# Optimization experiments

Hardware: AMD Instinct MI355X
Metric: run time of the kernel (lower is better)

Reference implementation:

```python
import jax, jax.numpy as jnp
import numpy as np
from jax import lax

NUM_BLOCKS = 8
BLOCK = 4  # hidden_size 32 // num_blocks 8
LAMBDA = 0.01  # sparsity_threshold
BN_EPS = 1e-5


def _bn(x, gamma, beta):
    # training-mode BatchNorm2d over (N, H, W) per channel
    mean = jnp.mean(x, axis=(0, 2, 3), keepdims=True)
    var = jnp.var(x, axis=(0, 2, 3), keepdims=True)
    return gamma[None, :, None, None] * (x - mean) * lax.rsqrt(var + BN_EPS) + beta[None, :, None, None]


def _softshrink(x, lam):
    return jnp.where(x > lam, x - lam, jnp.where(x < -lam, x + lam, jnp.zeros_like(x)))


def _afno(x, w1, b1, w2, b2):
    # AFNO2D_channelfirst: rfft2 -> block-diagonal complex 2-layer MLP -> softshrink
    # -> multiply with original spectrum -> irfft2 -> residual add
    B, C, H, W = x.shape
    bias = x
    xf = jnp.fft.rfft2(x, axes=(2, 3), norm="ortho")          # [B, C, H, W//2+1] complex
    orig = xf
    Wf = xf.shape[-1]
    xb = xf.reshape(B, NUM_BLOCKS, BLOCK, H, Wf)
    xr, xi = jnp.real(xb), jnp.imag(xb)
    # layer 1 (complex block matmul + bias + ReLU)
    o1r = jax.nn.relu(jnp.einsum('bkihw,kio->bkohw', xr, w1[0])
                      - jnp.einsum('bkihw,kio->bkohw', xi, w1[1])
                      + b1[0][None, :, :, None, None])
    o1i = jax.nn.relu(jnp.einsum('bkihw,kio->bkohw', xi, w1[0])
                      + jnp.einsum('bkihw,kio->bkohw', xr, w1[1])
                      + b1[1][None, :, :, None, None])
    # layer 2
    o2r = (jnp.einsum('bkihw,kio->bkohw', o1r, w2[0])
           - jnp.einsum('bkihw,kio->bkohw', o1i, w2[1])
           + b2[0][None, :, :, None, None])
    o2i = (jnp.einsum('bkihw,kio->bkohw', o1i, w2[0])
           + jnp.einsum('bkihw,kio->bkohw', o1r, w2[1])
           + b2[1][None, :, :, None, None])
    o2r = _softshrink(o2r, LAMBDA)
    o2i = _softshrink(o2i, LAMBDA)
    z = (o2r + 1j * o2i).reshape(B, C, H, Wf)
    z = z * orig                                              # spectral gating by original spectrum
    out = jnp.fft.irfft2(z, s=(H, W), axes=(2, 3), norm="ortho")
    return out + bias


def setup_inputs() -> dict:
    key = jax.random.key(0)
    ks = jax.random.split(key, 6)
    return {
        "x": jax.random.normal(ks[0], (4, 32, 512, 512), jnp.float32),
        "conv_w": jax.random.normal(ks[1], (32, 32, 3, 3), jnp.float32) * 0.05,
        "conv_b": jnp.zeros((32,), jnp.float32),
        "bn1_gamma": jnp.ones((32,), jnp.float32),
        "bn1_beta": jnp.zeros((32,), jnp.float32),
        "w1": jax.random.normal(ks[2], (2, NUM_BLOCKS, BLOCK, BLOCK), jnp.float32) * 0.02,
        "b1": jax.random.normal(ks[3], (2, NUM_BLOCKS, BLOCK), jnp.float32) * 0.02,
        "w2": jax.random.normal(ks[4], (2, NUM_BLOCKS, BLOCK, BLOCK), jnp.float32) * 0.02,
        "b2": jax.random.normal(ks[5], (2, NUM_BLOCKS, BLOCK), jnp.float32) * 0.02,
        "bn2_gamma": jnp.ones((32,), jnp.float32),
        "bn2_beta": jnp.zeros((32,), jnp.float32),
    }


def reference(x, conv_w, conv_b, bn1_gamma, bn1_beta, w1, b1, w2, b2, bn2_gamma, bn2_beta):
    # conv1 = Conv3x3(norm=True, act=True): conv 3x3 pad 1 + BN + ReLU
    y = lax.conv_general_dilated(x, conv_w, (1, 1), ((1, 1), (1, 1)),
                                 dimension_numbers=('NCHW', 'OIHW', 'NCHW'))
    y = y + conv_b[None, :, None, None]
    y = jax.nn.relu(_bn(y, bn1_gamma, bn1_beta))
    fo = _afno(y, w1, b1, w2, b2)
    fo = _bn(fo, bn2_gamma, bn2_beta)
    return jax.nn.relu(y + fo)
```

## Files before the change

### kernel.cpp

```cpp
#include <hip/hip_runtime.h>

#define WF 257
#define LAM 0.01f
#define ROWH 540
#define LPH(i) ((i) + (((i)>>6)<<2))

#define WSYNC() do { asm volatile("" ::: "memory"); __builtin_amdgcn_wave_barrier(); asm volatile("" ::: "memory"); } while(0)

typedef __attribute__((ext_vector_type(8))) short short8;
typedef __attribute__((ext_vector_type(4))) float f32x4;
typedef __attribute__((ext_vector_type(2))) __fp16 h2v;

__device__ __forceinline__ ushort f2bf(float f){
    unsigned u = __float_as_uint(f);
    unsigned r = (u + 0x7fffu + ((u >> 16) & 1u)) >> 16;
    return (ushort)r;
}
__device__ __forceinline__ float bf2f(ushort u){ return __uint_as_float((uint)u << 16); }
__device__ __forceinline__ uint packbf(float a, float b){
    return (uint)f2bf(a) | ((uint)f2bf(b) << 16);
}
__device__ __forceinline__ float2 unpackbf(uint u){
    return make_float2(__uint_as_float(u << 16), __uint_as_float(u & 0xffff0000u));
}
__device__ __forceinline__ uint packh(float a, float b){
    h2v h = __builtin_amdgcn_cvt_pkrtz(a, b);
    return *(uint*)&h;
}
__device__ __forceinline__ uint packh2(float2 v){ return packh(v.x, v.y); }
__device__ __forceinline__ float2 unph(uint u){
    h2v h = *(h2v*)&u;
    return make_float2((float)h[0], (float)h[1]);
}

__device__ __forceinline__ float2 cmul(float2 a, float2 b){
    return make_float2(a.x*b.x - a.y*b.y, a.x*b.y + a.y*b.x);
}
__device__ __forceinline__ float2 cadd(float2 a, float2 b){ return make_float2(a.x+b.x, a.y+b.y); }
__device__ __forceinline__ float2 csub(float2 a, float2 b){ return make_float2(a.x-b.x, a.y-b.y); }

template<int NTHREADS>
__device__ __forceinline__ void ld_tw(float2* tw, const float2* __restrict__ twg, int tid){
    for (int t = tid; t < 256; t += NTHREADS)
        ((float4*)tw)[t] = ((const float4*)twg)[t];
}

template<bool INV>
__device__ __forceinline__ float2 twz(const float2* tw, int idx){
    float2 w = tw[idx];
    if (INV) w.y = -w.y;
    return w;
}

template<bool INV>
__device__ __forceinline__ void dft8(float2 v[8]) {
    const float R = 0.70710678118654752f;
    float2 y0=v[0], y1=v[4], y2=v[2], y3=v[6], y4=v[1], y5=v[5], y6=v[3], y7=v[7];
    float2 t;
    t=y1; y1=csub(y0,t); y0=cadd(y0,t);
    t=y3; y3=csub(y2,t); y2=cadd(y2,t);
    t=y5; y5=csub(y4,t); y4=cadd(y4,t);
    t=y7; y7=csub(y6,t); y6=cadd(y6,t);
    t=y2; y2=csub(y0,t); y0=cadd(y0,t);
    t = INV ? make_float2(-y3.y, y3.x) : make_float2(y3.y, -y3.x);
    y3=csub(y1,t); y1=cadd(y1,t);
    t=y6; y6=csub(y4,t); y4=cadd(y4,t);
    t = INV ? make_float2(-y7.y, y7.x) : make_float2(y7.y, -y7.x);
    y7=csub(y5,t); y5=cadd(y5,t);
    t=y4; y4=csub(y0,t); y0=cadd(y0,t);
    { float2 w8 = INV ? make_float2(R, R) : make_float2(R,-R);
      t=cmul(y5,w8); y5=csub(y1,t); y1=cadd(y1,t); }
    t = INV ? make_float2(-y6.y, y6.x) : make_float2(y6.y, -y6.x);
    y6=csub(y2,t); y2=cadd(y2,t);
    { float2 w8 = INV ? make_float2(-R, R) : make_float2(-R,-R);
      t=cmul(y7,w8); y7=csub(y3,t); y3=cadd(y3,t); }
    v[0]=y0; v[1]=y1; v[2]=y2; v[3]=y3; v[4]=y4; v[5]=y5; v[6]=y6; v[7]=y7;
}

__device__ __forceinline__ void oct_write(uint* drow, int l, const float2 v[8]){
    uint* p = drow + LPH(8*l);
    *(uint4*)p       = make_uint4(packh2(v[0]), packh2(v[1]), packh2(v[2]), packh2(v[3]));
    *(uint4*)(p + 4) = make_uint4(packh2(v[4]), packh2(v[5]), packh2(v[6]), packh2(v[7]));
}

__device__ __forceinline__ void oct_gather(const uint* drow, int o0, float2 v[8]){
    const uint* b = drow + LPH(o0);
    #pragma unroll
    for (int q = 0; q < 8; ++q) v[q] = unph(b[68*q]);
}

template<bool INV>
__device__ __forceinline__ void fft_wave12(uint* drow, const float2* tw, int l)
{
    WSYNC();
    {
        int a = l&7, m = l>>3;
        uint* b = drow + 68*m + a;
        float2 v[8];
        v[0] = unph(b[0]);
        #pragma unroll
        for (int j = 1; j < 8; ++j)
            v[j] = cmul(unph(b[8*j]), twz<INV>(tw, 8*a*j));
        dft8<INV>(v);
        #pragma unroll
        for (int j = 0; j < 8; ++j) b[8*j] = packh2(v[j]);
    }
    WSYNC();
    {
        uint* b = drow + l;
        float2 v[8];
        v[0] = unph(b[0]);
        #pragma unroll
        for (int q = 1; q < 8; ++q)
            v[q] = cmul(unph(b[68*q]), twz<INV>(tw, (l*q)&511));
        dft8<INV>(v);
        #pragma unroll
        for (int q = 0; q < 8; ++q) b[68*q] = packh2(v[q]);
    }
    WSYNC();
}

__global__ void k_twiddle(float2* __restrict__ twg){
    int t = blockIdx.x*256 + threadIdx.x;
    if (t < 512) {
        float s, c;
        sincosf((float)t * (-6.2831853071795864769f/512.0f), &s, &c);
        twg[t] = make_float2(c, s);
    }
}

__global__ void k_wprep(const float* __restrict__ w, ushort* __restrict__ wtp){
    int i = blockIdx.x*256 + threadIdx.x;
    if (i < 9216) {
        int j = i & 7, l = (i>>3) & 63, m = (i>>9) & 1, tap = i >> 10;
        int co = m*16 + (l & 15), ci = ((l>>4)&3)*8 + j;
        wtp[i] = f2bf(w[(co*32 + ci)*9 + tap]);
    }
}

__global__ __launch_bounds__(256) void k_transpose(const float* __restrict__ x, ushort* __restrict__ xt){
    __shared__ ushort tl[64][36];
    const int tid = threadIdx.x;
    const int w0 = blockIdx.x*64, h = blockIdx.y, b = blockIdx.z;
    #pragma unroll
    for (int it = 0; it < 8; ++it) {
        int i = it*256 + tid, c = i >> 6, ww = i & 63;
        tl[ww][c] = f2bf(x[(((size_t)b*32 + c)*512 + h)*512 + w0 + ww]);
    }
    __syncthreads();
    const int ww = tid >> 2, c0 = (tid & 3) * 8;
    uint4 v;
    v.x = *(const uint*)&tl[ww][c0+0];
    v.y = *(const uint*)&tl[ww][c0+2];
    v.z = *(const uint*)&tl[ww][c0+4];
    v.w = *(const uint*)&tl[ww][c0+6];
    *(uint4*)(xt + ((((size_t)b*512 + h)*512 + w0 + ww)*32 + c0)) = v;
}

__global__ __launch_bounds__(256) void k_conv_mfma(
    const ushort* __restrict__ xt, const ushort* __restrict__ wtp,
    const float* __restrict__ bias, ushort* __restrict__ out, float* __restrict__ stats)
{
    __shared__ float sred[64];
    const int tid = threadIdx.x;
    const int wid = tid >> 6, lane = tid & 63;
    const int h = blockIdx.y*4 + wid;
    const int w0 = blockIdx.x*64;
    const int b = blockIdx.z;

    short8 wa[9][2];
    #pragma unroll
    for (int tap = 0; tap < 9; ++tap)
        #pragma unroll
        for (int m = 0; m < 2; ++m)
            wa[tap][m] = *reinterpret_cast<const short8*>(wtp + ((tap*2 + m)*64 + lane)*8);

    f32x4 acc[2][4];
    #pragma unroll
    for (int m = 0; m < 2; ++m)
        #pragma unroll
        for (int n = 0; n < 4; ++n)
            acc[m][n] = (f32x4){0.f, 0.f, 0.f, 0.f};

    const int c0 = ((lane >> 4) & 3) * 8;
    const int pw = w0 + (lane & 15);
    const size_t ibase = (size_t)b * 512 * 512;

    #pragma unroll
    for (int dy = -1; dy <= 1; ++dy) {
        const int hh = h + dy;
        const bool hok = (unsigned)hh < 512u;
        #pragma unroll
        for (int dx = -1; dx <= 1; ++dx) {
            const int tap = (dy+1)*3 + (dx+1);
            short8 bfr[4];
            #pragma unroll
            for (int n = 0; n < 4; ++n) {
                const int ww = pw + n*16 + dx;
                short8 v = {0,0,0,0,0,0,0,0};
                if (hok && (unsigned)ww < 512u)
                    v = *reinterpret_cast<const short8*>(xt + ((ibase + (size_t)hh*512 + ww)*32 + c0));
                bfr[n] = v;
            }
            #pragma unroll
            for (int m = 0; m < 2; ++m)
                #pragma unroll
                for (int n = 0; n < 4; ++n)
                    acc[m][n] = __builtin_amdgcn_mfma_f32_16x16x32_bf16(wa[tap][m], bfr[n], acc[m][n], 0, 0, 0);
        }
    }

    if (tid < 64) sred[tid] = 0.f;
    __syncthreads();

    float bv[2][4];
    #pragma unroll
    for (int m = 0; m < 2; ++m)
        #pragma unroll
        for (int r = 0; r < 4; ++r)
            bv[m][r] = bias[m*16 + ((lane>>4)&3)*4 + r];

    float s8[8], q8[8];
    #pragma unroll
    for (int i = 0; i < 8; ++i) { s8[i] = 0.f; q8[i] = 0.f; }

    #pragma unroll
    for (int m = 0; m < 2; ++m) {
        #pragma unroll
        for (int n = 0; n < 4; ++n) {
            #pragma unroll
            for (int r = 0; r < 4; ++r) {
                const int co = m*16 + ((lane>>4)&3)*4 + r;
                const int ww = w0 + n*16 + (lane & 15);
                float val = acc[m][n][r] + bv[m][r];
                out[(((size_t)b*32 + co)*512 + h)*512 + ww] = f2bf(val);
                s8[m*4+r] += val;
                q8[m*4+r] += val*val;
            }
        }
    }
    #pragma unroll
    for (int i = 0; i < 8; ++i) {
        #pragma unroll
        for (int off = 1; off < 16; off <<= 1) {
            s8[i] += __shfl_xor(s8[i], off, 64);
            q8[i] += __shfl_xor(q8[i], off, 64);
        }
    }
    if ((lane & 15) == 0) {
        #pragma unroll
        for (int m = 0; m < 2; ++m)
            #pragma unroll
            for (int r = 0; r < 4; ++r) {
                const int co = m*16 + ((lane>>4)&3)*4 + r;
                atomicAdd(&sred[co], s8[m*4+r]);
                atomicAdd(&sred[32+co], q8[m*4+r]);
            }
    }
    __syncthreads();
    if (tid < 64) {
        int bin = (blockIdx.y*8 + blockIdx.x + blockIdx.z) & 63;
        atomicAdd(&stats[bin*64 + tid], sred[tid]);
    }
}

__global__ void k_finalize(const float* __restrict__ stats, int nbins, const float* __restrict__ g,
                           const float* __restrict__ bta, float* __restrict__ bnp)
{
    int c = threadIdx.x;
    if (c < 32) {
        float s = 0.f, q = 0.f;
        for (int i = 0; i < nbins; ++i) { s += stats[i*64 + c]; q += stats[i*64 + 32 + c]; }
        const float inv_n = 1.f/1048576.f;
        float mean = s * inv_n;
        float var  = q * inv_n - mean*mean;
        float sc = g[c] * rsqrtf(var + 1e-5f);
        bnp[c] = sc;
        bnp[32+c] = bta[c] - mean*sc;
    }
}

__global__ void k_finalize2(const float* __restrict__ ystats, const float* __restrict__ sstats,
                            const float* __restrict__ g, const float* __restrict__ bta,
                            float* __restrict__ bnp2)
{
    int c = threadIdx.x;
    if (c < 32) {
        float Sy = 0.f, Sy2 = 0.f, Sgg = 0.f, Sgu = 0.f, Sg0 = 0.f;
        for (int i = 0; i < 64; ++i){ Sy  += ystats[i*64 + c]; Sy2 += ystats[i*64 + 32 + c]; }
        for (int i = 0; i < 32; ++i){ Sgg += sstats[i*96 + c]; Sgu += sstats[i*96 + 32 + c]; Sg0 += sstats[i*96 + 64 + c]; }
        const float inv_n = 1.f/1048576.f;
        float Sfo  = Sg0 + Sy;
        float Sfo2 = Sgg*(1.f/512.f) + Sgu*(2.f/512.f) + Sy2;
        float mean = Sfo*inv_n;
        float var  = Sfo2*inv_n - mean*mean;
        float sc = g[c]*rsqrtf(var + 1e-5f);
        bnp2[c] = sc;
        bnp2[32+c] = bta[c] - mean*sc;
    }
}

__global__ __launch_bounds__(512) void k_rowfft_fwd(
    const ushort* __restrict__ cvo, const float* __restrict__ bnp,
    const float2* __restrict__ twg, uint* __restrict__ spec, float* __restrict__ ystats)
{
    __shared__ float2 tw[512];
    __shared__ uint d[8*ROWH];
    const int tid = threadIdx.x;
    const int h0 = blockIdx.x * 16;
    const int bc = blockIdx.y;
    const int c = bc & 31;
    ld_tw<512>(tw, twg, tid);
    __syncthreads();
    const float s1 = bnp[c], t1 = bnp[32+c];
    const int row = tid >> 6, l = tid & 63;
    const int o0 = ((l&7)<<3) | (l>>3);
    uint* drow = d + row*ROWH;
    const ushort* rp0 = cvo + ((size_t)bc*512 + h0 + 2*row)*512 + o0;
    const ushort* rp1 = rp0 + 512;
    float ls = 0.f, lsq = 0.f;
    float2 v[8];
    #pragma unroll
    for (int q = 0; q < 8; ++q) {
        float y0 = fmaxf(fmaf(bf2f(rp0[64*q]), s1, t1), 0.f);
        float y1 = fmaxf(fmaf(bf2f(rp1[64*q]), s1, t1), 0.f);
        ls += y0 + y1; lsq += y0*y0 + y1*y1;
        v[q] = make_float2(y0, y1);
    }
    dft8<false>(v);
    oct_write(drow, l, v);
    fft_wave12<false>(drow, tw, l);
    __syncthreads();
    for (int i = tid; i < 8*WF; i += 512) {
        int p = i & 7, w = i >> 3;
        float2 Z  = unph(d[p*ROWH + LPH(w)]);
        float2 Zm = unph(d[p*ROWH + LPH((512 - w) & 511)]);
        float x1r = 0.5f*(Z.x + Zm.x), x1i = 0.5f*(Z.y - Zm.y);
        float x2r = 0.5f*(Z.y + Zm.y), x2i = 0.5f*(Zm.x - Z.x);
        uint2 pk;
        pk.x = packbf(x1r, x1i);
        pk.y = packbf(x2r, x2i);
        *(uint2*)(spec + ((size_t)bc*WF + w)*512 + h0 + 2*p) = pk;
    }
    #pragma unroll
    for (int off = 32; off; off >>= 1){ ls += __shfl_down(ls, off, 64); lsq += __shfl_down(lsq, off, 64); }
    if (l == 0) {
        int bin = ((blockIdx.x << 3) + row) & 63;
        atomicAdd(&ystats[bin*64 + c], ls);
        atomicAdd(&ystats[bin*64 + 32 + c], lsq);
    }
}

__global__ __launch_bounds__(512) void k_colfft(uint* __restrict__ spec,
    const float* __restrict__ w1, const float* __restrict__ b1,
    const float* __restrict__ w2, const float* __restrict__ b2,
    const float2* __restrict__ twg, float* __restrict__ sstats)
{
    __shared__ float2 tw[512];
    __shared__ uint d[8*ROWH];
    __shared__ float wl[160];
    const int tid = threadIdx.x;
    const int w = blockIdx.x;
    const int by = blockIdx.y;
    const int b = blockIdx.z;
    ld_tw<512>(tw, twg, tid);
    if (tid < 32) {
        int kg = tid >> 4, j = tid & 15;
        int k = by*2 + kg;
        wl[kg*80 + j]      = w1[k*16 + j];
        wl[kg*80 + 16 + j] = w1[128 + k*16 + j];
        wl[kg*80 + 32 + j] = w2[k*16 + j];
        wl[kg*80 + 48 + j] = w2[128 + k*16 + j];
    } else if (tid < 40) {
        int t = tid - 32, kg = t >> 2, o = t & 3;
        int k = by*2 + kg;
        wl[kg*80 + 64 + o] = b1[k*4 + o];
        wl[kg*80 + 68 + o] = b1[32 + k*4 + o];
        wl[kg*80 + 72 + o] = b2[k*4 + o];
        wl[kg*80 + 76 + o] = b2[32 + k*4 + o];
    }
    __syncthreads();
    const int cc = tid >> 6, l = tid & 63;
    const int o0 = ((l&7)<<3) | (l>>3);
    uint* drow = d + cc*ROWH;
    const size_t cbase = ((size_t)(b*32 + by*8 + cc)*WF + w) * 512;
    {
        const uint* sp = spec + cbase + o0;
        float2 v[8];
        #pragma unroll
        for (int q = 0; q < 8; ++q) {
            float2 u = unpackbf(sp[64*q]);
            v[q] = make_float2(u.x*(1.f/512.f), u.y*(1.f/512.f));
        }
        dft8<false>(v);
        oct_write(drow, l, v);
    }
    fft_wave12<false>(drow, tw, l);
    __syncthreads();
    const int ph = LPH(tid);
    #pragma unroll
    for (int kg = 0; kg < 2; ++kg) {
        const float* wk = wl + kg*80;
        const int rb = kg*4;
        float xr[4], xi[4];
        #pragma unroll
        for (int i = 0; i < 4; ++i) {
            float2 vv = unph(d[(rb+i)*ROWH + ph]);
            xr[i] = vv.x;
            xi[i] = vv.y;
        }
        float o1r[4], o1i[4];
        #pragma unroll
        for (int o = 0; o < 4; ++o) {
            float sr = wk[64+o], si = wk[68+o];
            #pragma unroll
            for (int i = 0; i < 4; ++i) {
                float wr = wk[i*4+o], wi = wk[16 + i*4+o];
                sr += xr[i]*wr - xi[i]*wi;
                si += xi[i]*wr + xr[i]*wi;
            }
            o1r[o] = fmaxf(sr, 0.f);
            o1i[o] = fmaxf(si, 0.f);
        }
        #pragma unroll
        for (int o = 0; o < 4; ++o) {
            float sr = wk[72+o], si = wk[76+o];
            #pragma unroll
            for (int i = 0; i < 4; ++i) {
                float wr = wk[32 + i*4+o], wi = wk[48 + i*4+o];
                sr += o1r[i]*wr - o1i[i]*wi;
                si += o1i[i]*wr + o1r[i]*wi;
            }
            sr = (sr > LAM) ? sr - LAM : ((sr < -LAM) ? sr + LAM : 0.f);
            si = (si > LAM) ? si - LAM : ((si < -LAM) ? si + LAM : 0.f);
            d[(rb+o)*ROWH + ph] = packh(sr*xr[o] - si*xi[o], sr*xi[o] + si*xr[o]);
        }
    }
    __syncthreads();
    {
        float2 v[8];
        oct_gather(drow, o0, v);
        dft8<true>(v);
        WSYNC();
        oct_write(drow, l, v);
    }
    fft_wave12<true>(drow, tw, l);
    const bool edge = (w == 0) || (w == 256);
    float fgg = 0.f, fgu = 0.f, fg0 = 0.f;
    #pragma unroll
    for (int it = 0; it < 4; ++it) {
        const int pos = it*64 + l;
        uint2 up = *(const uint2*)(spec + cbase + 2*pos);
        float2 u0 = unpackbf(up.x), u1 = unpackbf(up.y);
        uint2 dv = *(const uint2*)(drow + LPH(2*pos));
        float2 z0 = unph(dv.x), z1 = unph(dv.y);
        uint2 gp;
        gp.x = packbf(z0.x, z0.y);
        gp.y = packbf(z1.x, z1.y);
        *(uint2*)(spec + cbase + 2*pos) = gp;
        float2 g0 = unpackbf(gp.x), g1 = unpackbf(gp.y);
        if (edge) {
            fgg += g0.x*g0.x + g1.x*g1.x;
            fgu += g0.x*u0.x + g1.x*u1.x;
            if (w == 0) fg0 += g0.x + g1.x;
        } else {
            fgg += 2.f*(g0.x*g0.x + g0.y*g0.y + g1.x*g1.x + g1.y*g1.y);
            fgu += 2.f*(g0.x*u0.x + g0.y*u0.y + g1.x*u1.x + g1.y*u1.y);
        }
    }
    #pragma unroll
    for (int off = 32; off; off >>= 1){
        fgg += __shfl_down(fgg, off, 64);
        fgu += __shfl_down(fgu, off, 64);
        fg0 += __shfl_down(fg0, off, 64);
    }
    if (l == 0) {
        int kk = by*2 + (cc >> 2);
        int ch = cc & 3;
        int bin = (w + b*8 + kk) & 31;
        atomicAdd(&sstats[bin*96 + kk*4 + ch], fgg);
        atomicAdd(&sstats[bin*96 + 32 + kk*4 + ch], fgu);
        if (w == 0) atomicAdd(&sstats[bin*96 + 64 + kk*4 + ch], fg0);
    }
}

__global__ __launch_bounds__(512) void k_rowfft_inv(
    const uint* __restrict__ spec, const ushort* __restrict__ cvo,
    const float* __restrict__ bnp, const float* __restrict__ bnp2,
    const float2* __restrict__ twg, float* __restrict__ out)
{
    __shared__ float2 tw[512];
    __shared__ uint d[8*ROWH];
    const int tid = threadIdx.x;
    const int h0 = blockIdx.x * 16;
    const int bc = blockIdx.y;
    const int c = bc & 31;
    ld_tw<512>(tw, twg, tid);
    for (int i = tid; i < 8*WF; i += 512) {
        int p = i & 7, w = i >> 3;
        uint2 pk = *(const uint2*)(spec + ((size_t)bc*WF + w)*512 + h0 + 2*p);
        float2 X1 = unpackbf(pk.x), X2 = unpackbf(pk.y);
        if (w == 0 || w == 256) { X1.y = 0.f; X2.y = 0.f; }
        const float s = 1.f/512.f;
        d[p*ROWH + LPH(w)] = packh((X1.x - X2.y)*s, (X1.y + X2.x)*s);
        if ((unsigned)(w - 1) < 255u)
            d[p*ROWH + LPH(512 - w)] = packh((X1.x + X2.y)*s, (X2.x - X1.y)*s);
    }
    __syncthreads();
    const int row = tid >> 6, l = tid & 63;
    const int o0 = ((l&7)<<3) | (l>>3);
    uint* drow = d + row*ROWH;
    {
        float2 v[8];
        oct_gather(drow, o0, v);
        dft8<true>(v);
        WSYNC();
        oct_write(drow, l, v);
    }
    fft_wave12<true>(drow, tw, l);
    const float s1 = bnp[c],  t1 = bnp[32+c];
    const float s2 = bnp2[c], t2 = bnp2[32+c];
    const size_t gbase = ((size_t)bc*512 + h0 + 2*row)*512;
    #pragma unroll
    for (int q = 0; q < 8; ++q) {
        const int col = q*64 + l;
        float2 v = unph(drow[LPH(col)]);
        float y0 = fmaxf(fmaf(bf2f(cvo[gbase + col]), s1, t1), 0.f);
        float fo0 = v.x + y0;
        out[gbase + col] = fmaxf(y0 + fmaf(fo0, s2, t2), 0.f);
        float y1 = fmaxf(fmaf(bf2f(cvo[gbase + 512 + col]), s1, t1), 0.f);
        float fo1 = v.y + y1;
        out[gbase + 512 + col] = fmaxf(y1 + fmaf(fo1, s2, t2), 0.f);
    }
}

extern "C" void kernel_launch(void* const* d_in, const int* in_sizes, int n_in,
                              void* d_out, int out_size, void* d_ws, size_t ws_size,
                              hipStream_t stream)
{
    const float* x      = (const float*)d_in[0];
    const float* conv_w = (const float*)d_in[1];
    const float* conv_b = (const float*)d_in[2];
    const float* bn1g   = (const float*)d_in[3];
    const float* bn1b   = (const float*)d_in[4];
    const float* w1     = (const float*)d_in[5];
    const float* b1     = (const float*)d_in[6];
    const float* w2     = (const float*)d_in[7];
    const float* b2     = (const float*)d_in[8];
    const float* bn2g   = (const float*)d_in[9];
    const float* bn2b   = (const float*)d_in[10];
    float* out = (float*)d_out;

    char* ws = (char*)d_ws;
    uint*   spec  = (uint*)ws;
    ushort* xt    = (ushort*)ws;
    ushort* cvo   = (ushort*)(ws + 67371008);
    ushort* wtp   = (ushort*)(ws + 67371008 + 67108864);
    float*  stats = (float*)(ws + 67371008 + 67108864 + 18432);
    float* stats1 = stats;
    float* ystats = stats + 4096;
    float* sstats = stats + 8192;
    float* bnp1   = stats + 11264;
    float* bnp2   = stats + 11328;
    float2* twg   = (float2*)(stats + 11392);

    (void)hipMemsetAsync(stats, 0, 11264*sizeof(float), stream);
    k_twiddle<<<2, 256, 0, stream>>>(twg);
    k_wprep<<<36, 256, 0, stream>>>(conv_w, wtp);
    k_transpose<<<dim3(8,512,4), 256, 0, stream>>>(x, xt);
    k_conv_mfma<<<dim3(8,128,4), 256, 0, stream>>>(xt, wtp, conv_b, cvo, stats1);
    k_finalize<<<1, 64, 0, stream>>>(stats1, 64, bn1g, bn1b, bnp1);
    k_rowfft_fwd<<<dim3(32,128), 512, 0, stream>>>(cvo, bnp1, twg, spec, ystats);
    k_colfft<<<dim3(257,4,4), 512, 0, stream>>>(spec, w1, b1, w2, b2, twg, sstats);
    k_finalize2<<<1, 64, 0, stream>>>(ystats, sstats, bn2g, bn2b, bnp2);
    k_rowfft_inv<<<dim3(32,128), 512, 0, stream>>>(spec, cvo, bnp1, bnp2, twg, out);
}
```

Before: 357.7 us.

## Compute column FFTs as fp16 MFMA DFT matmuls over all 32 channels per block

Replaces the radix-8 shared-memory column FFT in k_colfft with a two-stage 16x32 decomposition done as complex DFT matrix multiplies on fp16 MFMA units, forward and inverse. Each block now handles all 32 channels of one frequency column, so the grid shrinks from 257x4x4 to 257x4 and the block-MLP runs over all 8 channel groups at once. The aim is to move butterfly arithmetic and the twiddle and permutation shuffles onto matrix cores. In exchange it uses about 66 KB of LDS per block, which lowers occupancy, has half-idle lanes in the 16-point stage, and adds fp16 rounding inside the DFT.

```diff
diff --git a/kernel.cpp b/kernel.cpp
--- a/kernel.cpp
+++ b/kernel.cpp
@@ -10,6 +10,9 @@
 typedef __attribute__((ext_vector_type(8))) short short8;
 typedef __attribute__((ext_vector_type(4))) float f32x4;
 typedef __attribute__((ext_vector_type(2))) __fp16 h2v;
+typedef __attribute__((ext_vector_type(8))) __fp16 h8;
+
+union UH8 { uint4 u; h8 h; };
 
 __device__ __forceinline__ ushort f2bf(float f){
     unsigned u = __float_as_uint(f);
@@ -356,58 +359,153 @@
     const float* __restrict__ w2, const float* __restrict__ b2,
     const float2* __restrict__ twg, float* __restrict__ sstats)
 {
+    __shared__ uint sl[32*513];
     __shared__ float2 tw[512];
-    __shared__ uint d[8*ROWH];
-    __shared__ float wl[160];
+    __shared__ float wl[640];
     const int tid = threadIdx.x;
-    const int w = blockIdx.x;
-    const int by = blockIdx.y;
-    const int b = blockIdx.z;
-    ld_tw<512>(tw, twg, tid);
-    if (tid < 32) {
-        int kg = tid >> 4, j = tid & 15;
-        int k = by*2 + kg;
-        wl[kg*80 + j]      = w1[k*16 + j];
-        wl[kg*80 + 16 + j] = w1[128 + k*16 + j];
-        wl[kg*80 + 32 + j] = w2[k*16 + j];
-        wl[kg*80 + 48 + j] = w2[128 + k*16 + j];
-    } else if (tid < 40) {
-        int t = tid - 32, kg = t >> 2, o = t & 3;
-        int k = by*2 + kg;
-        wl[kg*80 + 64 + o] = b1[k*4 + o];
-        wl[kg*80 + 68 + o] = b1[32 + k*4 + o];
-        wl[kg*80 + 72 + o] = b2[k*4 + o];
-        wl[kg*80 + 76 + o] = b2[32 + k*4 + o];
-    }
-    __syncthreads();
-    const int cc = tid >> 6, l = tid & 63;
-    const int o0 = ((l&7)<<3) | (l>>3);
-    uint* drow = d + cc*ROWH;
-    const size_t cbase = ((size_t)(b*32 + by*8 + cc)*WF + w) * 512;
+    const int lane = tid & 63, wv = tid >> 6;
+    const int w = blockIdx.x, b = blockIdx.y;
+    const int l15 = lane & 15, lq = lane >> 4;
+    const int kb = lq * 8;
+
+    for (int t = tid; t < 256; t += 512)
+        ((float4*)tw)[t] = ((const float4*)twg)[t];
+    if (tid < 128) {
+        int g = tid >> 4, j = tid & 15;
+        wl[g*80 + j]      = w1[g*16 + j];
+        wl[g*80 + 16 + j] = w1[128 + g*16 + j];
+        wl[g*80 + 32 + j] = w2[g*16 + j];
+        wl[g*80 + 48 + j] = w2[128 + g*16 + j];
+    } else if (tid < 160) {
+        int t2 = tid - 128, g = t2 >> 2, o = t2 & 3;
+        wl[g*80 + 64 + o] = b1[g*4 + o];
+        wl[g*80 + 68 + o] = b1[32 + g*4 + o];
+        wl[g*80 + 72 + o] = b2[g*4 + o];
+        wl[g*80 + 76 + o] = b2[32 + g*4 + o];
+    }
+    const size_t gbase = ((size_t)b*32*WF + w) * 512;
+    #pragma unroll 4
+    for (int c = 0; c < 32; ++c) {
+        float2 u = unpackbf(spec[gbase + (size_t)c*(WF*512) + tid]);
+        sl[c*513 + tid] = packh(u.x*(1.f/512.f), u.y*(1.f/512.f));
+    }
+    __syncthreads();
+
     {
-        const uint* sp = spec + cbase + o0;
-        float2 v[8];
-        #pragma unroll
-        for (int q = 0; q < 8; ++q) {
-            float2 u = unpackbf(sp[64*q]);
-            v[q] = make_float2(u.x*(1.f/512.f), u.y*(1.f/512.f));
-        }
-        dft8<false>(v);
-        oct_write(drow, l, v);
-    }
-    fft_wave12<false>(drow, tw, l);
-    __syncthreads();
-    const int ph = LPH(tid);
-    #pragma unroll
-    for (int kg = 0; kg < 2; ++kg) {
-        const float* wk = wl + kg*80;
-        const int rb = kg*4;
+        h8 Fr[2], Fi[2], nFi[2];
+        #pragma unroll
+        for (int mt = 0; mt < 2; ++mt) {
+            const int m = mt*16 + l15;
+            uint ur[4], ui[4], un[4];
+            #pragma unroll
+            for (int p = 0; p < 4; ++p) {
+                float2 t0 = tw[(16*m*(kb + 2*p)) & 511];
+                float2 t1 = tw[(16*m*(kb + 2*p+1)) & 511];
+                ur[p] = packh(t0.x, t1.x);
+                ui[p] = packh(t0.y, t1.y);
+                un[p] = ui[p] ^ 0x80008000u;
+            }
+            UH8 a; a.u = make_uint4(ur[0],ur[1],ur[2],ur[3]); Fr[mt]=a.h;
+            UH8 bb; bb.u = make_uint4(ui[0],ui[1],ui[2],ui[3]); Fi[mt]=bb.h;
+            UH8 cc; cc.u = make_uint4(un[0],un[1],un[2],un[3]); nFi[mt]=cc.h;
+        }
+        #pragma unroll
+        for (int s = 0; s < 2; ++s) {
+            const int n1 = wv*2 + s;
+            h8 Br[2], Bi[2];
+            #pragma unroll
+            for (int nt = 0; nt < 2; ++nt) {
+                const int base = (nt*16 + l15)*513 + n1;
+                uint dd[8];
+                #pragma unroll
+                for (int j = 0; j < 8; ++j) dd[j] = sl[base + 16*(kb + j)];
+                uint br[4], bi[4];
+                #pragma unroll
+                for (int p = 0; p < 4; ++p) {
+                    br[p] = (dd[2*p] & 0xffffu) | (dd[2*p+1] << 16);
+                    bi[p] = (dd[2*p] >> 16) | (dd[2*p+1] & 0xffff0000u);
+                }
+                UH8 t1_; t1_.u = make_uint4(br[0],br[1],br[2],br[3]); Br[nt]=t1_.h;
+                UH8 t2_; t2_.u = make_uint4(bi[0],bi[1],bi[2],bi[3]); Bi[nt]=t2_.h;
+            }
+            #pragma unroll
+            for (int mt = 0; mt < 2; ++mt)
+            #pragma unroll
+            for (int nt = 0; nt < 2; ++nt) {
+                f32x4 yr = {0.f,0.f,0.f,0.f}, yi = {0.f,0.f,0.f,0.f};
+                yr = __builtin_amdgcn_mfma_f32_16x16x32_f16(Fr[mt], Br[nt], yr, 0,0,0);
+                yr = __builtin_amdgcn_mfma_f32_16x16x32_f16(nFi[mt], Bi[nt], yr, 0,0,0);
+                yi = __builtin_amdgcn_mfma_f32_16x16x32_f16(Fr[mt], Bi[nt], yi, 0,0,0);
+                yi = __builtin_amdgcn_mfma_f32_16x16x32_f16(Fi[mt], Br[nt], yi, 0,0,0);
+                const int cw = (nt*16 + l15)*513 + n1;
+                #pragma unroll
+                for (int r = 0; r < 4; ++r)
+                    sl[cw + 16*(mt*16 + lq*4 + r)] = packh(yr[r], yi[r]);
+            }
+        }
+    }
+    __syncthreads();
+
+    #pragma unroll
+    for (int s = 0; s < 4; ++s) {
+        const int k2 = wv*4 + s;
+        h8 Ar, Ai, nAi;
+        {
+            uint ar[4]={0,0,0,0}, ai[4]={0,0,0,0}, an[4]={0,0,0,0};
+            if (lane < 32) {
+                const int kk = k2 + 32*l15;
+                #pragma unroll
+                for (int p = 0; p < 4; ++p) {
+                    float2 t0 = tw[((kb + 2*p)*kk) & 511];
+                    float2 t1 = tw[((kb + 2*p+1)*kk) & 511];
+                    ar[p] = packh(t0.x, t1.x);
+                    ai[p] = packh(t0.y, t1.y);
+                    an[p] = ai[p] ^ 0x80008000u;
+                }
+            }
+            UH8 a; a.u = make_uint4(ar[0],ar[1],ar[2],ar[3]); Ar=a.h;
+            UH8 bb; bb.u = make_uint4(ai[0],ai[1],ai[2],ai[3]); Ai=bb.h;
+            UH8 cc; cc.u = make_uint4(an[0],an[1],an[2],an[3]); nAi=cc.h;
+        }
+        #pragma unroll
+        for (int ct = 0; ct < 2; ++ct) {
+            const int cb2 = (ct*16 + l15)*513 + 16*k2;
+            h8 Br, Bi;
+            {
+                uint dd[8] = {0,0,0,0,0,0,0,0};
+                if (lane < 32) {
+                    #pragma unroll
+                    for (int j = 0; j < 8; ++j) dd[j] = sl[cb2 + kb + j];
+                }
+                uint br[4], bi[4];
+                #pragma unroll
+                for (int p = 0; p < 4; ++p) {
+                    br[p] = (dd[2*p] & 0xffffu) | (dd[2*p+1] << 16);
+                    bi[p] = (dd[2*p] >> 16) | (dd[2*p+1] & 0xffff0000u);
+                }
+                UH8 t1_; t1_.u = make_uint4(br[0],br[1],br[2],br[3]); Br=t1_.h;
+                UH8 t2_; t2_.u = make_uint4(bi[0],bi[1],bi[2],bi[3]); Bi=t2_.h;
+            }
+            f32x4 xr = {0.f,0.f,0.f,0.f}, xi = {0.f,0.f,0.f,0.f};
+            xr = __builtin_amdgcn_mfma_f32_16x16x32_f16(Ar, Br, xr, 0,0,0);
+            xr = __builtin_amdgcn_mfma_f32_16x16x32_f16(nAi, Bi, xr, 0,0,0);
+            xi = __builtin_amdgcn_mfma_f32_16x16x32_f16(Ar, Bi, xi, 0,0,0);
+            xi = __builtin_amdgcn_mfma_f32_16x16x32_f16(Ai, Br, xi, 0,0,0);
+            #pragma unroll
+            for (int r = 0; r < 4; ++r)
+                sl[cb2 + lq*4 + r] = packh(xr[r], xi[r]);
+        }
+    }
+    __syncthreads();
+
+    #pragma unroll
+    for (int g = 0; g < 8; ++g) {
+        const float* wk = wl + g*80;
         float xr[4], xi[4];
         #pragma unroll
         for (int i = 0; i < 4; ++i) {
-            float2 vv = unph(d[(rb+i)*ROWH + ph]);
-            xr[i] = vv.x;
-            xi[i] = vv.y;
+            float2 v = unph(sl[(4*g+i)*513 + tid]);
+            xr[i] = v.x; xi[i] = v.y;
         }
         float o1r[4], o1i[4];
         #pragma unroll
@@ -433,54 +531,159 @@
             }
             sr = (sr > LAM) ? sr - LAM : ((sr < -LAM) ? sr + LAM : 0.f);
             si = (si > LAM) ? si - LAM : ((si < -LAM) ? si + LAM : 0.f);
-            d[(rb+o)*ROWH + ph] = packh(sr*xr[o] - si*xi[o], sr*xi[o] + si*xr[o]);
-        }
-    }
-    __syncthreads();
+            sl[(4*g+o)*513 + tid] = packh(sr*xr[o] - si*xi[o], sr*xi[o] + si*xr[o]);
+        }
+    }
+    __syncthreads();
+
     {
-        float2 v[8];
-        oct_gather(drow, o0, v);
-        dft8<true>(v);
-        WSYNC();
-        oct_write(drow, l, v);
-    }
-    fft_wave12<true>(drow, tw, l);
+        h8 Gr, Gi, nGi;
+        {
+            uint gr[4]={0,0,0,0}, gi[4]={0,0,0,0}, gn[4]={0,0,0,0};
+            if (lane < 32) {
+                #pragma unroll
+                for (int p = 0; p < 4; ++p) {
+                    float2 t0 = tw[(32*(kb + 2*p)*l15) & 511];
+                    float2 t1 = tw[(32*(kb + 2*p+1)*l15) & 511];
+                    gr[p] = packh(t0.x, t1.x);
+                    gi[p] = packh(-t0.y, -t1.y);
+                    gn[p] = gi[p] ^ 0x80008000u;
+                }
+            }
+            UH8 a; a.u = make_uint4(gr[0],gr[1],gr[2],gr[3]); Gr=a.h;
+            UH8 bb; bb.u = make_uint4(gi[0],gi[1],gi[2],gi[3]); Gi=bb.h;
+            UH8 cc; cc.u = make_uint4(gn[0],gn[1],gn[2],gn[3]); nGi=cc.h;
+        }
+        #pragma unroll
+        for (int s = 0; s < 4; ++s) {
+            const int k2 = wv*4 + s;
+            #pragma unroll
+            for (int ct = 0; ct < 2; ++ct) {
+                const int cb2 = (ct*16 + l15)*513 + 16*k2;
+                h8 Br, Bi;
+                {
+                    uint dd[8] = {0,0,0,0,0,0,0,0};
+                    if (lane < 32) {
+                        #pragma unroll
+                        for (int j = 0; j < 8; ++j) dd[j] = sl[cb2 + kb + j];
+                    }
+                    uint br[4], bi[4];
+                    #pragma unroll
+                    for (int p = 0; p < 4; ++p) {
+                        br[p] = (dd[2*p] & 0xffffu) | (dd[2*p+1] << 16);
+                        bi[p] = (dd[2*p] >> 16) | (dd[2*p+1] & 0xffff0000u);
+                    }
+                    UH8 t1_; t1_.u = make_uint4(br[0],br[1],br[2],br[3]); Br=t1_.h;
+                    UH8 t2_; t2_.u = make_uint4(bi[0],bi[1],bi[2],bi[3]); Bi=t2_.h;
+                }
+                f32x4 yr = {0.f,0.f,0.f,0.f}, yi = {0.f,0.f,0.f,0.f};
+                yr = __builtin_amdgcn_mfma_f32_16x16x32_f16(Gr, Br, yr, 0,0,0);
+                yr = __builtin_amdgcn_mfma_f32_16x16x32_f16(nGi, Bi, yr, 0,0,0);
+                yi = __builtin_amdgcn_mfma_f32_16x16x32_f16(Gr, Bi, yi, 0,0,0);
+                yi = __builtin_amdgcn_mfma_f32_16x16x32_f16(Gi, Br, yi, 0,0,0);
+                #pragma unroll
+                for (int r = 0; r < 4; ++r)
+                    sl[cb2 + lq*4 + r] = packh(yr[r], yi[r]);
+            }
+        }
+    }
+    __syncthreads();
+
+    #pragma unroll
+    for (int s = 0; s < 2; ++s) {
+        const int n1 = wv*2 + s;
+        h8 Cr[2], Ci[2], nCi[2];
+        #pragma unroll
+        for (int mt = 0; mt < 2; ++mt) {
+            const int hh = n1 + 16*(mt*16 + l15);
+            uint cr[4], ci[4], cn[4];
+            #pragma unroll
+            for (int p = 0; p < 4; ++p) {
+                float2 t0 = tw[(hh*(kb + 2*p)) & 511];
+                float2 t1 = tw[(hh*(kb + 2*p+1)) & 511];
+                cr[p] = packh(t0.x, t1.x);
+                ci[p] = packh(-t0.y, -t1.y);
+                cn[p] = ci[p] ^ 0x80008000u;
+            }
+            UH8 a; a.u = make_uint4(cr[0],cr[1],cr[2],cr[3]); Cr[mt]=a.h;
+            UH8 bb; bb.u = make_uint4(ci[0],ci[1],ci[2],ci[3]); Ci[mt]=bb.h;
+            UH8 cc; cc.u = make_uint4(cn[0],cn[1],cn[2],cn[3]); nCi[mt]=cc.h;
+        }
+        h8 Br[2], Bi[2];
+        #pragma unroll
+        for (int nt = 0; nt < 2; ++nt) {
+            const int base = (nt*16 + l15)*513 + n1;
+            uint dd[8];
+            #pragma unroll
+            for (int j = 0; j < 8; ++j) dd[j] = sl[base + 16*(kb + j)];
+            uint br[4], bi[4];
+            #pragma unroll
+            for (int p = 0; p < 4; ++p) {
+                br[p] = (dd[2*p] & 0xffffu) | (dd[2*p+1] << 16);
+                bi[p] = (dd[2*p] >> 16) | (dd[2*p+1] & 0xffff0000u);
+            }
+            UH8 t1_; t1_.u = make_uint4(br[0],br[1],br[2],br[3]); Br[nt]=t1_.h;
+            UH8 t2_; t2_.u = make_uint4(bi[0],bi[1],bi[2],bi[3]); Bi[nt]=t2_.h;
+        }
+        #pragma unroll
+        for (int mt = 0; mt < 2; ++mt)
+        #pragma unroll
+        for (int nt = 0; nt < 2; ++nt) {
+            f32x4 xr = {0.f,0.f,0.f,0.f}, xi = {0.f,0.f,0.f,0.f};
+            xr = __builtin_amdgcn_mfma_f32_16x16x32_f16(Cr[mt], Br[nt], xr, 0,0,0);
+            xr = __builtin_amdgcn_mfma_f32_16x16x32_f16(nCi[mt], Bi[nt], xr, 0,0,0);
+            xi = __builtin_amdgcn_mfma_f32_16x16x32_f16(Cr[mt], Bi[nt], xi, 0,0,0);
+            xi = __builtin_amdgcn_mfma_f32_16x16x32_f16(Ci[mt], Br[nt], xi, 0,0,0);
+            const int cw = (nt*16 + l15)*513 + n1;
+            #pragma unroll
+            for (int r = 0; r < 4; ++r)
+                sl[cw + 16*(mt*16 + lq*4 + r)] = packh(xr[r], xi[r]);
+        }
+    }
+    __syncthreads();
+
     const bool edge = (w == 0) || (w == 256);
-    float fgg = 0.f, fgu = 0.f, fg0 = 0.f;
-    #pragma unroll
-    for (int it = 0; it < 4; ++it) {
-        const int pos = it*64 + l;
-        uint2 up = *(const uint2*)(spec + cbase + 2*pos);
-        float2 u0 = unpackbf(up.x), u1 = unpackbf(up.y);
-        uint2 dv = *(const uint2*)(drow + LPH(2*pos));
-        float2 z0 = unph(dv.x), z1 = unph(dv.y);
-        uint2 gp;
-        gp.x = packbf(z0.x, z0.y);
-        gp.y = packbf(z1.x, z1.y);
-        *(uint2*)(spec + cbase + 2*pos) = gp;
-        float2 g0 = unpackbf(gp.x), g1 = unpackbf(gp.y);
-        if (edge) {
-            fgg += g0.x*g0.x + g1.x*g1.x;
-            fgu += g0.x*u0.x + g1.x*u1.x;
-            if (w == 0) fg0 += g0.x + g1.x;
-        } else {
-            fgg += 2.f*(g0.x*g0.x + g0.y*g0.y + g1.x*g1.x + g1.y*g1.y);
-            fgu += 2.f*(g0.x*u0.x + g0.y*u0.y + g1.x*u1.x + g1.y*u1.y);
-        }
-    }
-    #pragma unroll
-    for (int off = 32; off; off >>= 1){
-        fgg += __shfl_down(fgg, off, 64);
-        fgu += __shfl_down(fgu, off, 64);
-        fg0 += __shfl_down(fg0, off, 64);
-    }
-    if (l == 0) {
-        int kk = by*2 + (cc >> 2);
-        int ch = cc & 3;
-        int bin = (w + b*8 + kk) & 31;
-        atomicAdd(&sstats[bin*96 + kk*4 + ch], fgg);
-        atomicAdd(&sstats[bin*96 + 32 + kk*4 + ch], fgu);
-        if (w == 0) atomicAdd(&sstats[bin*96 + 64 + kk*4 + ch], fg0);
+    #pragma unroll
+    for (int i = 0; i < 4; ++i) {
+        const int c = wv*4 + i;
+        const size_t cb = gbase + (size_t)c*(WF*512);
+        float fgg = 0.f, fgu = 0.f, fg0 = 0.f;
+        #pragma unroll
+        for (int it = 0; it < 4; ++it) {
+            const int pos = it*128 + 2*lane;
+            uint2 dv;
+            dv.x = sl[c*513 + pos];
+            dv.y = sl[c*513 + pos + 1];
+            float2 z0 = unph(dv.x), z1 = unph(dv.y);
+            uint2 up = *(const uint2*)(spec + cb + pos);
+            float2 u0 = unpackbf(up.x), u1 = unpackbf(up.y);
+            uint2 gp;
+            gp.x = packbf(z0.x, z0.y);
+            gp.y = packbf(z1.x, z1.y);
+            *(uint2*)(spec + cb + pos) = gp;
+            float2 g0 = unpackbf(gp.x), g1 = unpackbf(gp.y);
+            if (edge) {
+                fgg += g0.x*g0.x + g1.x*g1.x;
+                fgu += g0.x*u0.x + g1.x*u1.x;
+                if (w == 0) fg0 += g0.x + g1.x;
+            } else {
+                fgg += 2.f*(g0.x*g0.x + g0.y*g0.y + g1.x*g1.x + g1.y*g1.y);
+                fgu += 2.f*(g0.x*u0.x + g0.y*u0.y + g1.x*u1.x + g1.y*u1.y);
+            }
+        }
+        #pragma unroll
+        for (int off = 32; off; off >>= 1){
+            fgg += __shfl_down(fgg, off, 64);
+            fgu += __shfl_down(fgu, off, 64);
+            fg0 += __shfl_down(fg0, off, 64);
+        }
+        if (lane == 0) {
+            const int kk = c >> 2, ch = c & 3;
+            const int bin = (w + b*8 + kk) & 31;
+            atomicAdd(&sstats[bin*96 + kk*4 + ch], fgg);
+            atomicAdd(&sstats[bin*96 + 32 + kk*4 + ch], fgu);
+            if (w == 0) atomicAdd(&sstats[bin*96 + 64 + kk*4 + ch], fg0);
+        }
     }
 }
 
@@ -571,7 +774,7 @@
     k_conv_mfma<<<dim3(8,128,4), 256, 0, stream>>>(xt, wtp, conv_b, cvo, stats1);
     k_finalize<<<1, 64, 0, stream>>>(stats1, 64, bn1g, bn1b, bnp1);
     k_rowfft_fwd<<<dim3(32,128), 512, 0, stream>>>(cvo, bnp1, twg, spec, ystats);
-    k_colfft<<<dim3(257,4,4), 512, 0, stream>>>(spec, w1, b1, w2, b2, twg, sstats);
+    k_colfft<<<dim3(257,4), 512, 0, stream>>>(spec, w1, b1, w2, b2, twg, sstats);
     k_finalize2<<<1, 64, 0, stream>>>(ystats, sstats, bn2g, bn2b, bnp2);
     k_rowfft_inv<<<dim3(32,128), 512, 0, stream>>>(spec, cvo, bnp1, bnp2, twg, out);
 }
```

Result: faster. 330.7 us (-7.5%).
